# Performance work log

Hardware: AMD Instinct MI355X
Metric: run time of the kernel (lower is better)

Reference implementation:

```python
import jax, jax.numpy as jnp
import numpy as np

HIDDEN = 512
BATCH = 32
SEQ = 4096


def setup_inputs() -> dict:
    key = jax.random.key(0)
    ks = jax.random.split(key, 8)
    s = 1.0 / np.sqrt(HIDDEN)
    return {
        "encoder_outputs": jax.random.normal(ks[0], (BATCH, SEQ, HIDDEN), jnp.float32),
        "decoder_hidden": jax.random.normal(ks[1], (BATCH, HIDDEN), jnp.float32),
        "W_enc": jax.random.uniform(ks[2], (HIDDEN, HIDDEN), jnp.float32, -s, s),
        "b_enc": jax.random.uniform(ks[3], (HIDDEN,), jnp.float32, -s, s),
        "W_dec": jax.random.uniform(ks[4], (HIDDEN, HIDDEN), jnp.float32, -s, s),
        "b_dec": jax.random.uniform(ks[5], (HIDDEN,), jnp.float32, -s, s),
        "W_v": jax.random.uniform(ks[6], (HIDDEN, 1), jnp.float32, -s, s),
        "b_v": jax.random.uniform(ks[7], (1,), jnp.float32, -s, s),
    }


def reference(encoder_outputs, decoder_hidden, W_enc, b_enc, W_dec, b_dec, W_v, b_v):
    # (b, s, h) projected encoder states
    enc_proj = jnp.einsum("bsh,hk->bsk", encoder_outputs, W_enc) + b_enc
    # (b, 1, h) projected decoder state, broadcast-added over seq
    dec_proj = (decoder_hidden @ W_dec + b_dec)[:, None, :]
    # score: (b, s, 1)
    score = jnp.tanh(enc_proj + dec_proj) @ W_v + b_v
    attention_weights = jax.nn.softmax(score, axis=1)  # softmax over seq_len
    # context: (b, h) weighted sum of encoder outputs
    context = jnp.sum(attention_weights * encoder_outputs, axis=1)
    return context, jnp.squeeze(attention_weights, -1)
```

## Files before the change

kernel.cpp:

```cpp
#include <hip/hip_runtime.h>
#include <hip/hip_bf16.h>

typedef __attribute__((ext_vector_type(8))) short bf16x8;
typedef __attribute__((ext_vector_type(4))) float f32x4;

#define HID 512
#define NB 32
#define SEQL 4096
#define BM 32
#define NBLK 4096

#define WS_BP    0
#define WS_DPROJ (512*1024)
#define WS_SUM   (576*1024)

__device__ __forceinline__ short f2bf(float f) {
    unsigned u = __float_as_uint(f);
    unsigned r = (u + 0x7fffu + ((u >> 16) & 1u)) >> 16;
    return (short)r;
}

__device__ __forceinline__ float fast_tanh(float x) {
    float e = __expf(2.0f * x);
    float r = __builtin_amdgcn_rcpf(e + 1.0f);
    return 1.0f - 2.0f * r;
}

__device__ __forceinline__ unsigned cvtpk(float lo, float hi) {
    unsigned r;
    asm("v_cvt_pk_bf16_f32 %0, %1, %2" : "=v"(r) : "v"(lo), "v"(hi));
    return r;
}
__device__ __forceinline__ bf16x8 pack8(const float4& A, const float4& B) {
    union { unsigned u[4]; bf16x8 v; } t;
    t.u[0] = cvtpk(A.x, A.y); t.u[1] = cvtpk(A.z, A.w);
    t.u[2] = cvtpk(B.x, B.y); t.u[3] = cvtpk(B.z, B.w);
    return t.v;
}

__global__ void k_pre(const float* __restrict__ We, short* __restrict__ Bp,
                      const float* __restrict__ dec, const float* __restrict__ Wd,
                      const float* __restrict__ be, const float* __restrict__ bd,
                      float* __restrict__ dproj, float* __restrict__ out,
                      float* __restrict__ sumacc) {
    const int blk = blockIdx.x, t = threadIdx.x;
    if (blk < 128) {
        int tid  = blk * 256 + t;
        int lane = tid & 63;
        int nt   = (tid >> 6) & 31;
        int kc   = tid >> 11;
        int k0   = kc * 32 + (lane >> 4) * 8;
        int n    = nt * 16 + (lane & 15);
        bf16x8 v;
#pragma unroll
        for (int j = 0; j < 8; ++j) v[j] = f2bf(We[(size_t)(k0 + j) * HID + n]);
        *(bf16x8*)&Bp[(size_t)tid * 8] = v;
    } else if (blk < 640) {
        __shared__ float red[8][33];
        int bid2 = blk - 128;
        int b  = bid2 >> 4, kg = bid2 & 15;
        int kl = t & 31,    hc = t >> 5;
        int k  = kg * 32 + kl;
        const float* dr = dec + (size_t)b * HID;
        float a = 0.f;
#pragma unroll 8
        for (int j = 0; j < 64; ++j) {
            int h = hc * 64 + j;
            a += dr[h] * Wd[(size_t)h * HID + k];
        }
        red[hc][kl] = a;
        __syncthreads();
        if (hc == 0) {
            float s = be[k] + bd[k];
#pragma unroll
            for (int c = 0; c < 8; ++c) s += red[c][kl];
            dproj[(size_t)b * HID + k] = s;
        }
    } else {
        int bz = blk - 640;
        out[bz * 256 + t] = 0.f;
        if (bz == 0 && t < NB) sumacc[t] = 0.f;
    }
}

__global__ __launch_bounds__(256, 3)
void k_main(const float* __restrict__ E, const short* __restrict__ Bp,
            const float* __restrict__ dproj, const float* __restrict__ Wv,
            float* __restrict__ out, float* __restrict__ sumacc) {
    __shared__ float fbuf[512];
    __shared__ float pbuf[BM];

    const int tid  = threadIdx.x;
    const int wave = tid >> 6, lane = tid & 63;
    const int quad = lane >> 4, l15 = lane & 15;
    const int bid  = blockIdx.x;
    const int row0 = bid * BM;
    const int b    = bid >> 7;
    const int stag = bid & 15;

    f32x4 acc[2][8];
#pragma unroll
    for (int r = 0; r < 2; ++r)
#pragma unroll
        for (int c = 0; c < 8; ++c) acc[r][c] = (f32x4){0.f, 0.f, 0.f, 0.f};

    const float* a0p = E + (size_t)(row0 + l15) * HID + quad * 8;
    const float* a1p = E + (size_t)(row0 + 16 + l15) * HID + quad * 8;
    const short* bpw = Bp + ((size_t)(wave * 8) * 64 + lane) * 8;

    int kcs = stag;
    float4 a00 = *(const float4*)(a0p + kcs * 32);
    float4 a01 = *(const float4*)(a0p + kcs * 32 + 4);
    float4 a10 = *(const float4*)(a1p + kcs * 32);
    float4 a11 = *(const float4*)(a1p + kcs * 32 + 4);

    for (int kc = 0; kc < 16; ++kc) {
        const short* bsrc = bpw + (size_t)kcs * 16384;
        bf16x8 fb[8];
#pragma unroll
        for (int c = 0; c < 8; ++c)
            fb[c] = *(const bf16x8*)(bsrc + c * 512);
        const int kn = (kcs + 1) & 15;
        float4 n00, n01, n10, n11;
        if (kc < 15) {
            n00 = *(const float4*)(a0p + kn * 32);
            n01 = *(const float4*)(a0p + kn * 32 + 4);
            n10 = *(const float4*)(a1p + kn * 32);
            n11 = *(const float4*)(a1p + kn * 32 + 4);
        }
        bf16x8 fa0 = pack8(a00, a01);
        bf16x8 fa1 = pack8(a10, a11);
#pragma unroll
        for (int c = 0; c < 8; ++c) {
            acc[0][c] = __builtin_amdgcn_mfma_f32_16x16x32_bf16(fa0, fb[c], acc[0][c], 0, 0, 0);
            acc[1][c] = __builtin_amdgcn_mfma_f32_16x16x32_bf16(fa1, fb[c], acc[1][c], 0, 0, 0);
        }
        if (kc < 15) { a00 = n00; a01 = n01; a10 = n10; a11 = n11; }
        kcs = kn;
    }

    float part[2][4];
#pragma unroll
    for (int r = 0; r < 2; ++r)
#pragma unroll
        for (int g = 0; g < 4; ++g) part[r][g] = 0.f;
    const float* dp = dproj + (size_t)b * HID;
#pragma unroll
    for (int c = 0; c < 8; ++c) {
        int col = wave * 128 + c * 16 + l15;
        float dv = dp[col];
        float wv = Wv[col];
#pragma unroll
        for (int r = 0; r < 2; ++r)
#pragma unroll
            for (int g = 0; g < 4; ++g)
                part[r][g] += fast_tanh(acc[r][c][g] + dv) * wv;
    }
#pragma unroll
    for (int r = 0; r < 2; ++r)
#pragma unroll
        for (int g = 0; g < 4; ++g) {
            float v = part[r][g];
            v += __shfl_xor(v, 1); v += __shfl_xor(v, 2);
            v += __shfl_xor(v, 4); v += __shfl_xor(v, 8);
            part[r][g] = v;
        }
    if (l15 == 0) {
#pragma unroll
        for (int r = 0; r < 2; ++r)
#pragma unroll
            for (int g = 0; g < 4; ++g)
                fbuf[wave * 32 + r * 16 + quad * 4 + g] = part[r][g];
    }
    __syncthreads();
    if (tid < 32) {
        float s  = fbuf[tid] + fbuf[32 + tid] + fbuf[64 + tid] + fbuf[96 + tid];
        float pv = __expf(s);
        pbuf[tid] = pv;
        out[(size_t)NB * HID + row0 + tid] = pv;
        float t2 = pv;
        t2 += __shfl_xor(t2, 1); t2 += __shfl_xor(t2, 2); t2 += __shfl_xor(t2, 4);
        t2 += __shfl_xor(t2, 8); t2 += __shfl_xor(t2, 16);
        if (tid == 0) atomicAdd(&sumacc[b], t2);
    }
    __syncthreads();

    const int hq = tid & 127, rh = tid >> 7;
    const float4* E4 = (const float4*)E;
    size_t cbase = (size_t)(row0 + rh * 16) * (HID / 4) + hq;
    float4 ca = {0.f, 0.f, 0.f, 0.f};
#pragma unroll 4
    for (int rr = 0; rr < 16; ++rr) {
        float w  = pbuf[rh * 16 + rr];
        float4 e = E4[cbase + (size_t)rr * (HID / 4)];
        ca.x += w * e.x; ca.y += w * e.y; ca.z += w * e.z; ca.w += w * e.w;
    }
    if (rh == 1) {
        fbuf[hq] = ca.x; fbuf[128 + hq] = ca.y; fbuf[256 + hq] = ca.z; fbuf[384 + hq] = ca.w;
    }
    __syncthreads();
    if (rh == 0) {
        ca.x += fbuf[hq]; ca.y += fbuf[128 + hq]; ca.z += fbuf[256 + hq]; ca.w += fbuf[384 + hq];
        float* cg = out + (size_t)b * HID + hq * 4;
        atomicAdd(cg + 0, ca.x); atomicAdd(cg + 1, ca.y);
        atomicAdd(cg + 2, ca.z); atomicAdd(cg + 3, ca.w);
    }
}

__global__ void k_finish(float* __restrict__ out, const float* __restrict__ sumacc) {
    int idx = blockIdx.x * 256 + threadIdx.x;
    if (idx < NB * HID) {
        out[idx] *= 1.0f / sumacc[idx >> 9];
    } else {
        int w = idx - NB * HID;
        out[idx] *= 1.0f / sumacc[w >> 12];
    }
}

extern "C" void kernel_launch(void* const* d_in, const int* in_sizes, int n_in,
                              void* d_out, int out_size, void* d_ws, size_t ws_size,
                              hipStream_t stream) {
    const float* E   = (const float*)d_in[0];
    const float* dec = (const float*)d_in[1];
    const float* We  = (const float*)d_in[2];
    const float* be  = (const float*)d_in[3];
    const float* Wd  = (const float*)d_in[4];
    const float* bd  = (const float*)d_in[5];
    const float* Wv  = (const float*)d_in[6];
    float* out = (float*)d_out;
    char*  ws  = (char*)d_ws;
    short* Bp     = (short*)(ws + WS_BP);
    float* dproj  = (float*)(ws + WS_DPROJ);
    float* sumacc = (float*)(ws + WS_SUM);

    k_pre<<<704, 256, 0, stream>>>(We, Bp, dec, Wd, be, bd, dproj, out, sumacc);
    k_main<<<NBLK, 256, 0, stream>>>(E, Bp, dproj, Wv, out, sumacc);
    k_finish<<<576, 256, 0, stream>>>(out, sumacc);
}
```

Before: 544.1 us.

## Stage encoder tile as bf16 in LDS and split B-fragment loads into halves

Each block now loads its 32x512 encoder tile with coalesced float4 reads, converts it to bf16 once, and stores it in a padded LDS array. A-fragments are then read from LDS instead of strided global loads. The B-fragment loads are split into two half-batches that are double-buffered against the MFMAs, and the K loop is fully unrolled. Occupancy is raised to 4 blocks per CU, which adds about 33KB of LDS per block and more register pressure.

```diff
diff --git a/kernel.cpp b/kernel.cpp
--- a/kernel.cpp
+++ b/kernel.cpp
@@ -3,6 +3,7 @@
 
 typedef __attribute__((ext_vector_type(8))) short bf16x8;
 typedef __attribute__((ext_vector_type(4))) float f32x4;
+typedef __attribute__((ext_vector_type(4))) short s16x4;
 
 #define HID 512
 #define NB 32
@@ -30,12 +31,6 @@
     unsigned r;
     asm("v_cvt_pk_bf16_f32 %0, %1, %2" : "=v"(r) : "v"(lo), "v"(hi));
     return r;
-}
-__device__ __forceinline__ bf16x8 pack8(const float4& A, const float4& B) {
-    union { unsigned u[4]; bf16x8 v; } t;
-    t.u[0] = cvtpk(A.x, A.y); t.u[1] = cvtpk(A.z, A.w);
-    t.u[2] = cvtpk(B.x, B.y); t.u[3] = cvtpk(B.z, B.w);
-    return t.v;
 }
 
 __global__ void k_pre(const float* __restrict__ We, short* __restrict__ Bp,
@@ -83,10 +78,11 @@
     }
 }
 
-__global__ __launch_bounds__(256, 3)
+__global__ __launch_bounds__(256, 4)
 void k_main(const float* __restrict__ E, const short* __restrict__ Bp,
             const float* __restrict__ dproj, const float* __restrict__ Wv,
             float* __restrict__ out, float* __restrict__ sumacc) {
+    __shared__ short As[BM][520];
     __shared__ float fbuf[512];
     __shared__ float pbuf[BM];
 
@@ -98,46 +94,60 @@
     const int b    = bid >> 7;
     const int stag = bid & 15;
 
+    {
+        const float4* src4 = (const float4*)(E + (size_t)(row0 + wave * 8) * HID);
+#pragma unroll
+        for (int i = 0; i < 16; ++i) {
+            float4 v = src4[i * 64 + lane];
+            int fo  = i * 256 + lane * 4;
+            int r8  = fo >> 9;
+            int col = fo & 511;
+            union { unsigned u[2]; s16x4 s; } t;
+            t.u[0] = cvtpk(v.x, v.y);
+            t.u[1] = cvtpk(v.z, v.w);
+            *(s16x4*)&As[wave * 8 + r8][col] = t.s;
+        }
+    }
+    __syncthreads();
+
     f32x4 acc[2][8];
 #pragma unroll
     for (int r = 0; r < 2; ++r)
 #pragma unroll
         for (int c = 0; c < 8; ++c) acc[r][c] = (f32x4){0.f, 0.f, 0.f, 0.f};
 
-    const float* a0p = E + (size_t)(row0 + l15) * HID + quad * 8;
-    const float* a1p = E + (size_t)(row0 + 16 + l15) * HID + quad * 8;
     const short* bpw = Bp + ((size_t)(wave * 8) * 64 + lane) * 8;
 
-    int kcs = stag;
-    float4 a00 = *(const float4*)(a0p + kcs * 32);
-    float4 a01 = *(const float4*)(a0p + kcs * 32 + 4);
-    float4 a10 = *(const float4*)(a1p + kcs * 32);
-    float4 a11 = *(const float4*)(a1p + kcs * 32 + 4);
-
+#define LOADB4(dst, kk, c0) do {                                         \
+        const short* bsrc_ = bpw + (size_t)(kk) * 16384 + (c0) * 512;    \
+        _Pragma("unroll")                                                \
+        for (int c_ = 0; c_ < 4; ++c_)                                   \
+            dst[c_] = *(const bf16x8*)(bsrc_ + c_ * 512);                \
+    } while (0)
+
+    bf16x8 fbA[4], fbB[4];
+    LOADB4(fbA, stag, 0);
+#pragma unroll
     for (int kc = 0; kc < 16; ++kc) {
-        const short* bsrc = bpw + (size_t)kcs * 16384;
-        bf16x8 fb[8];
-#pragma unroll
-        for (int c = 0; c < 8; ++c)
-            fb[c] = *(const bf16x8*)(bsrc + c * 512);
-        const int kn = (kcs + 1) & 15;
-        float4 n00, n01, n10, n11;
-        if (kc < 15) {
-            n00 = *(const float4*)(a0p + kn * 32);
-            n01 = *(const float4*)(a0p + kn * 32 + 4);
-            n10 = *(const float4*)(a1p + kn * 32);
-            n11 = *(const float4*)(a1p + kn * 32 + 4);
-        }
-        bf16x8 fa0 = pack8(a00, a01);
-        bf16x8 fa1 = pack8(a10, a11);
-#pragma unroll
-        for (int c = 0; c < 8; ++c) {
-            acc[0][c] = __builtin_amdgcn_mfma_f32_16x16x32_bf16(fa0, fb[c], acc[0][c], 0, 0, 0);
-            acc[1][c] = __builtin_amdgcn_mfma_f32_16x16x32_bf16(fa1, fb[c], acc[1][c], 0, 0, 0);
-        }
-        if (kc < 15) { a00 = n00; a01 = n01; a10 = n10; a11 = n11; }
-        kcs = kn;
-    }
+        const int kcs = (stag + kc) & 15;
+        LOADB4(fbB, kcs, 4);
+        bf16x8 fa[2];
+#pragma unroll
+        for (int r = 0; r < 2; ++r)
+            fa[r] = *(bf16x8*)&As[r * 16 + l15][kcs * 32 + quad * 8];
+#pragma unroll
+        for (int c = 0; c < 4; ++c)
+#pragma unroll
+            for (int r = 0; r < 2; ++r)
+                acc[r][c] = __builtin_amdgcn_mfma_f32_16x16x32_bf16(fa[r], fbA[c], acc[r][c], 0, 0, 0);
+        if (kc < 15) LOADB4(fbA, (kcs + 1) & 15, 0);
+#pragma unroll
+        for (int c = 0; c < 4; ++c)
+#pragma unroll
+            for (int r = 0; r < 2; ++r)
+                acc[r][c + 4] = __builtin_amdgcn_mfma_f32_16x16x32_bf16(fa[r], fbB[c], acc[r][c + 4], 0, 0, 0);
+    }
+#undef LOADB4
 
     float part[2][4];
 #pragma unroll
@@ -174,7 +184,7 @@
     }
     __syncthreads();
     if (tid < 32) {
-        float s  = fbuf[tid] + fbuf[32 + tid] + fbuf[64 + tid] + fbuf[96 + tid];
+        float s = fbuf[tid] + fbuf[32 + tid] + fbuf[64 + tid] + fbuf[96 + tid];
         float pv = __expf(s);
         pbuf[tid] = pv;
         out[(size_t)NB * HID + row0 + tid] = pv;
```

New measurement: 483.8 us. 1.12x faster.
